# Optimization experiments

Hardware: AMD Instinct MI355X
Metric: run time of the kernel (lower is better)

The kernel has to match this reference:

```python
import jax, jax.numpy as jnp
import numpy as np

GD, LD, HEAD, P, K = 64, 64, 8, 8, 3
GH = HEAD * GD // (GD + LD)   # 4 global heads
LH = HEAD - GH                # 4 local heads
CG = GD // GH                 # 16 = global head dim
CL = LD // LH                 # 16 = local per-head channels
C = GD + LD
EPS = 1e-5


def setup_inputs() -> dict:
    key = jax.random.key(0)
    ks = jax.random.split(key, 16)
    s = 0.02
    inp = {
        'x': jax.random.normal(ks[0], (32, C, 64, 64), jnp.float32),
        'norm_g': jnp.ones((C,), jnp.float32),
        'norm_b': jnp.zeros((C,), jnp.float32),
        'fc1_w': jax.random.normal(ks[1], (3 * GD, GD), jnp.float32) * s,
        'fc1_b': jnp.zeros((3 * GD,), jnp.float32),
        'fc2_w': jax.random.normal(ks[2], (3 * LD, LD), jnp.float32) * s,
        'fc2_b': jnp.zeros((3 * LD,), jnp.float32),
        'qconv_w': jax.random.normal(ks[3], (CL, 1, K, K), jnp.float32) * s,
        'qconv_b': jnp.zeros((CL,), jnp.float32),
        'kconv_w': jax.random.normal(ks[4], (CL, 1, K, K), jnp.float32) * s,
        'kconv_b': jnp.zeros((CL,), jnp.float32),
        'vconv_w': jax.random.normal(ks[5], (CL, 1, K, K), jnp.float32) * s,
        'vconv_b': jnp.zeros((CL,), jnp.float32),
        'fc3_w': jax.random.normal(ks[6], (CL, CL), jnp.float32) * s,
        'fc3_b': jnp.zeros((CL,), jnp.float32),
        'fc4_w': jax.random.normal(ks[7], (CL, CL), jnp.float32) * s,
        'fc4_b': jnp.zeros((CL,), jnp.float32),
        'fc5_w': jax.random.normal(ks[8], (C, C), jnp.float32) * s,
        'fc5_b': jnp.zeros((C,), jnp.float32),
    }
    return inp


def _layernorm(x, g, b):
    m = x.mean(-1, keepdims=True)
    v = ((x - m) ** 2).mean(-1, keepdims=True)
    return (x - m) / jnp.sqrt(v + EPS) * g + b


def _dwconv(x, w, b):
    # x: [N, CL, H, W], w: [CL, 1, K, K] depthwise
    y = jax.lax.conv_general_dilated(
        x, w, (1, 1), [(K // 2, K // 2), (K // 2, K // 2)],
        dimension_numbers=('NCHW', 'OIHW', 'NCHW'), feature_group_count=w.shape[0])
    return y + b[None, :, None, None]


def _conv1x1(x, w, b):
    return jnp.einsum('oc,bchw->bohw', w, x) + b[None, :, None, None]


def reference(x, norm_g, norm_b, fc1_w, fc1_b, fc2_w, fc2_b,
              qconv_w, qconv_b, kconv_w, kconv_b, vconv_w, vconv_b,
              fc3_w, fc3_b, fc4_w, fc4_b, fc5_w, fc5_b):
    B, Cc, H, W = x.shape
    N = H * W
    xn = x.transpose(0, 2, 3, 1).reshape(B, N, Cc)          # b (h w) c
    xn = _layernorm(xn, norm_g, norm_b)
    x_local, x_global = xn[..., :LD], xn[..., LD:]

    # ----- global branch: pooled-KV softmax attention -----
    gqkv = x_global @ fc1_w.T + fc1_b                        # [B,N,3GD]
    gqkv = gqkv.reshape(B, N, 3, GH, CG).transpose(2, 0, 3, 1, 4)  # [3,B,GH,N,CG]
    gq, gk, gv = gqkv[0], gqkv[1], gqkv[2]

    def pool_kv(t):
        t = t.reshape(B, GH, H, W, CG).transpose(0, 1, 4, 2, 3)      # [B,GH,CG,H,W]
        t = t.reshape(B, GH, CG, H // P, P, W // P, P).mean((4, 6))  # avg-pool P
        return t.transpose(0, 1, 3, 4, 2).reshape(B, GH, (H // P) * (W // P), CG)

    gk, gv = pool_kv(gk), pool_kv(gv)
    attn = jnp.einsum('bhnc,bhmc->bhnm', gq, gk) * (GD ** -0.5)  # [B,GH,N,Np]
    attn = jax.nn.softmax(attn, axis=-1)
    xg = jnp.einsum('bhnm,bhmc->bhnc', attn, gv)
    xg = xg.reshape(B, GH, H, W, CG).transpose(0, 1, 4, 2, 3).reshape(B, GD, H, W)

    # ----- local branch: depthwise-conv QKV with swish/tanh gating -----
    lqkv = x_local @ fc2_w.T + fc2_b                          # [B,N,3LD]
    lqkv = lqkv.reshape(B, H, W, 3, LH, CL).transpose(3, 0, 4, 5, 1, 2)
    lqkv = lqkv.reshape(3, B * LH, CL, H, W)
    lq = _dwconv(lqkv[0], qconv_w, qconv_b)
    lk = _dwconv(lqkv[1], kconv_w, kconv_b)
    lv = _dwconv(lqkv[2], vconv_w, vconv_b)
    a = lq * lk
    a = _conv1x1(a, fc3_w, fc3_b)
    a = jax.nn.silu(a)
    a = _conv1x1(a, fc4_w, fc4_b)
    a = jnp.tanh(a / (LD ** -0.5))
    xl = (a * lv).reshape(B, LD, H, W)

    xc = jnp.concatenate([xl, xg], axis=1)                    # [B,C,H,W]
    out = x + _conv1x1(xc, fc5_w, fc5_b)
    return out
```

## Files before the change

### kernel.cpp

```cpp
#include <hip/hip_runtime.h>
#include <cstddef>

#define HW 4096
#define PL 4752
#define RS 72
#define APL (2048 * 4752)

typedef short bf16x8 __attribute__((ext_vector_type(8)));
typedef unsigned short u16x8 __attribute__((ext_vector_type(8)));
typedef float f32x4 __attribute__((ext_vector_type(4)));
typedef unsigned int u32x4 __attribute__((ext_vector_type(4)));
typedef unsigned int u32x2 __attribute__((ext_vector_type(2)));

__device__ __forceinline__ unsigned short f2bf(float f) {
    unsigned u = __builtin_bit_cast(unsigned, f);
    u += 0x7fffu + ((u >> 16) & 1u);
    return (unsigned short)(u >> 16);
}
__device__ __forceinline__ float bf2f(unsigned short s) {
    return __builtin_bit_cast(float, ((unsigned)s) << 16);
}
__device__ __forceinline__ float dpp_left(float x) {
    return __builtin_bit_cast(float,
        __builtin_amdgcn_update_dpp(0, __builtin_bit_cast(int, x), 0x138, 0xf, 0xf, false));
}
__device__ __forceinline__ float dpp_right(float x) {
    return __builtin_bit_cast(float,
        __builtin_amdgcn_update_dpp(0, __builtin_bit_cast(int, x), 0x130, 0xf, 0xf, false));
}

__global__ __launch_bounds__(256) void kprep(
    const float* __restrict__ w1, const float* __restrict__ w2, const float* __restrict__ w5,
    const float* __restrict__ b1, const float* __restrict__ b2,
    unsigned short* __restrict__ wcat, unsigned short* __restrict__ wb5,
    float* __restrict__ bcat)
{
    const int i = blockIdx.x * 256 + threadIdx.x;
    if (i < 384 * 64) {
        const int r = i >> 6;
        wcat[i] = f2bf(r < 192 ? w2[i] : w1[i - 192 * 64]);
    }
    if (i < 128 * 128) wb5[i] = f2bf(w5[i]);
    if (i < 384) bcat[i] = (i < 192) ? b2[i] : b1[i - 192];
}

__global__ __launch_bounds__(256) void kzero(unsigned short* __restrict__ lqkv)
{
    unsigned short* plane = lqkv + (size_t)blockIdx.x * PL;
    const int i = threadIdx.x;
    if (i < 144) {
        const int r = (i < 72) ? 0 : 65;
        plane[r * RS + (i % 72)] = 0;
    }
}

__global__ __launch_bounds__(256) void k1_ln_fc(
    const float* __restrict__ x, const float* __restrict__ ng, const float* __restrict__ nb,
    const unsigned short* __restrict__ wcat, const float* __restrict__ bcat,
    unsigned short* __restrict__ gqb, float* __restrict__ gkp, float* __restrict__ gvp,
    unsigned short* __restrict__ lqkv)
{
    __shared__ unsigned short xnT[64 * 128];
    __shared__ float red[2][4][64];
    const int t = threadIdx.x;
    const int g = t >> 6;
    const int p = t & 63;
    const int bx = blockIdx.x;
    const int b = bx >> 6;
    const int h = bx & 63;
    const float* xrow = x + (size_t)b * 128 * HW + h * 64;

    float v[32];
    float s1 = 0.f, s2 = 0.f;
    #pragma unroll
    for (int i = 0; i < 32; ++i) {
        const int c = g * 32 + i;
        const float vv = xrow[(size_t)c * HW + p];
        v[i] = vv; s1 += vv; s2 += vv * vv;
    }
    red[0][g][p] = s1; red[1][g][p] = s2;
    __syncthreads();
    const float m   = (red[0][0][p] + red[0][1][p] + red[0][2][p] + red[0][3][p]) * (1.f / 128.f);
    const float var = (red[1][0][p] + red[1][1][p] + red[1][2][p] + red[1][3][p]) * (1.f / 128.f) - m * m;
    const float rstd = rsqrtf(var + 1e-5f);

    #pragma unroll
    for (int j = 0; j < 4; ++j) {
        u32x4 pk;
        #pragma unroll
        for (int q = 0; q < 4; ++q) {
            const int i0 = j * 8 + q * 2;
            const int c0 = g * 32 + i0;
            const float f0 = (v[i0]     - m) * rstd * ng[c0]     + nb[c0];
            const float f1 = (v[i0 + 1] - m) * rstd * ng[c0 + 1] + nb[c0 + 1];
            pk[q] = (unsigned)f2bf(f0) | ((unsigned)f2bf(f1) << 16);
        }
        const int colu = (g * 32 + j * 8) ^ ((p & 7) * 8);
        *reinterpret_cast<u32x4*>(&xnT[p * 128 + colu]) = pk;
    }
    __syncthreads();

    const int wid = g;
    const int lg = p >> 4, lr = p & 15;
    const int kbase = (wid >= 2) ? 64 : 0;

    bf16x8 afr[4][2];
    #pragma unroll
    for (int mt = 0; mt < 4; ++mt)
        #pragma unroll
        for (int kc = 0; kc < 2; ++kc) {
            const int pix = mt * 16 + lr;
            const int colu = (kbase + kc * 32 + lg * 8) ^ ((pix & 7) * 8);
            afr[mt][kc] = *reinterpret_cast<const bf16x8*>(&xnT[pix * 128 + colu]);
        }

    const int nbase = wid * 96;
    #pragma unroll
    for (int nt = 0; nt < 6; ++nt) {
        const int o0 = nbase + nt * 16;
        const int o  = o0 + lr;
        const float bias = bcat[o];
        f32x4 acc[4];
        #pragma unroll
        for (int mt = 0; mt < 4; ++mt) acc[mt] = f32x4{bias, bias, bias, bias};
        #pragma unroll
        for (int kc = 0; kc < 2; ++kc) {
            const bf16x8 bfr = *reinterpret_cast<const bf16x8*>(&wcat[(size_t)o * 64 + kc * 32 + lg * 8]);
            #pragma unroll
            for (int mt = 0; mt < 4; ++mt)
                acc[mt] = __builtin_amdgcn_mfma_f32_16x16x32_bf16(afr[mt][kc], bfr, acc[mt], 0, 0, 0);
        }
        if (o0 < 192) {
            const int cc = o0 >> 6;
            const int lh2 = (o0 & 63) >> 4;
            unsigned short* dst = lqkv + (size_t)cc * APL
                                + (((size_t)b * 4 + lh2) * 16 + lr) * PL
                                + (size_t)(h + 1) * RS + 4;
            #pragma unroll
            for (int mt = 0; mt < 4; ++mt) {
                u32x2 pk;
                pk[0] = (unsigned)f2bf(acc[mt][0]) | ((unsigned)f2bf(acc[mt][1]) << 16);
                pk[1] = (unsigned)f2bf(acc[mt][2]) | ((unsigned)f2bf(acc[mt][3]) << 16);
                *reinterpret_cast<u32x2*>(&dst[mt * 16 + lg * 4]) = pk;
            }
        } else if (o0 < 256) {
            const int gh = (o0 - 192) >> 4;
            unsigned short* dst = gqb + (((size_t)b * 4 + gh) * 16) * HW;
            #pragma unroll
            for (int mt = 0; mt < 4; ++mt) {
                u32x2 pk;
                pk[0] = (unsigned)f2bf(acc[mt][0]) | ((unsigned)f2bf(acc[mt][1]) << 16);
                pk[1] = (unsigned)f2bf(acc[mt][2]) | ((unsigned)f2bf(acc[mt][3]) << 16);
                *reinterpret_cast<u32x2*>(&dst[(size_t)lr * HW + h * 64 + mt * 16 + lg * 4]) = pk;
            }
        } else {
            const int kvsel = (o0 - 256) >> 6;
            const int gh = ((o0 - 256) & 63) >> 4;
            float* dst = (kvsel ? gvp : gkp) + (((size_t)b * 4 + gh) * 64 + (h >> 3) * 8) * 16;
            #pragma unroll
            for (int mt = 0; mt < 4; ++mt) {
                float s = acc[mt][0] + acc[mt][1] + acc[mt][2] + acc[mt][3];
                s += __shfl_xor(s, 16);
                if (!(p & 16))
                    atomicAdd(&dst[(2 * mt + (lg >> 1)) * 16 + lr], s * (1.f / 64.f));
            }
        }
    }
}

__global__ __launch_bounds__(256) void k2_attn(
    const unsigned short* __restrict__ gqb, const float* __restrict__ gkp,
    const float* __restrict__ gvp, unsigned short* __restrict__ xc)
{
    __shared__ float skv[2][64][16];
    const int t = threadIdx.x;
    const int bx = blockIdx.x;
    const int tile = bx & 15;
    const int bg = bx >> 4;
    const int b = bg >> 2;
    const int gh = bg & 3;
    for (int i = t; i < 1024; i += 256) {
        skv[0][i >> 4][i & 15] = gkp[(size_t)bg * 1024 + i];
        skv[1][i >> 4][i & 15] = gvp[(size_t)bg * 1024 + i];
    }
    __syncthreads();
    const int n = tile * 256 + t;
    const unsigned short* qp = gqb + (size_t)bg * 16 * HW + n;
    float q[16];
    #pragma unroll
    for (int cg = 0; cg < 16; ++cg) q[cg] = bf2f(qp[(size_t)cg * HW]) * 0.125f;
    float s[64];
    #pragma unroll
    for (int mm = 0; mm < 64; ++mm) {
        float a = 0.f;
        #pragma unroll
        for (int cg = 0; cg < 16; ++cg) a = fmaf(q[cg], skv[0][mm][cg], a);
        s[mm] = a;
    }
    float mx = s[0];
    #pragma unroll
    for (int mm = 1; mm < 64; ++mm) mx = fmaxf(mx, s[mm]);
    float sum = 0.f;
    #pragma unroll
    for (int mm = 0; mm < 64; ++mm) { float e = __expf(s[mm] - mx); s[mm] = e; sum += e; }
    const float rs = 1.f / sum;
    float acc[16];
    #pragma unroll
    for (int cg = 0; cg < 16; ++cg) acc[cg] = 0.f;
    #pragma unroll
    for (int mm = 0; mm < 64; ++mm) {
        const float pm = s[mm];
        #pragma unroll
        for (int cg = 0; cg < 16; ++cg) acc[cg] = fmaf(pm, skv[1][mm][cg], acc[cg]);
    }
    unsigned short* op = xc + ((size_t)b * 128 + 64 + gh * 16) * HW + n;
    #pragma unroll
    for (int cg = 0; cg < 16; ++cg) op[(size_t)cg * HW] = f2bf(acc[cg] * rs);
}

__global__ __launch_bounds__(256, 4) void k3_local(
    const unsigned short* __restrict__ lqkv,
    const float* __restrict__ qw, const float* __restrict__ qb,
    const float* __restrict__ kw, const float* __restrict__ kb,
    const float* __restrict__ vw, const float* __restrict__ vb,
    const float* __restrict__ w3, const float* __restrict__ b3,
    const float* __restrict__ w4, const float* __restrict__ b4,
    unsigned short* __restrict__ xc)
{
    const int t = threadIdx.x;
    const int w = t & 63;
    const int rr = t >> 6;
    const int bx = blockIdx.x;
    const int htile = bx & 15;
    const int bl = bx >> 4;
    const int b = bl >> 2;
    const int lh = bl & 3;
    const int h = htile * 4 + rr;

    float a[16], lvv[16];
    #pragma unroll
    for (int cl = 0; cl < 16; ++cl) {
        const size_t pb = ((size_t)bl * 16 + cl) * PL + (size_t)h * RS + 4 + w;
        float aq = qb[cl], ak = kb[cl], av = vb[cl];
        #pragma unroll
        for (int dy = 0; dy < 3; ++dy) {
            const size_t idx = pb + (size_t)dy * RS;
            const float cq = bf2f(lqkv[idx]);
            const float ck = bf2f(lqkv[idx + APL]);
            const float cv = bf2f(lqkv[idx + 2 * APL]);
            const float lq = dpp_left(cq),  rq = dpp_right(cq);
            const float lk = dpp_left(ck),  rk = dpp_right(ck);
            const float lv = dpp_left(cv),  rv = dpp_right(cv);
            const int wi = cl * 9 + dy * 3;
            aq = fmaf(qw[wi], lq, aq); aq = fmaf(qw[wi + 1], cq, aq); aq = fmaf(qw[wi + 2], rq, aq);
            ak = fmaf(kw[wi], lk, ak); ak = fmaf(kw[wi + 1], ck, ak); ak = fmaf(kw[wi + 2], rk, ak);
            av = fmaf(vw[wi], lv, av); av = fmaf(vw[wi + 1], cv, av); av = fmaf(vw[wi + 2], rv, av);
        }
        a[cl] = aq * ak;
        lvv[cl] = av;
    }

    float a2[16];
    #pragma unroll
    for (int o = 0; o < 16; ++o) {
        float acc = b3[o];
        #pragma unroll
        for (int c2 = 0; c2 < 16; ++c2) acc = fmaf(w3[o * 16 + c2], a[c2], acc);
        a2[o] = acc / (1.f + __expf(-acc));
    }
    unsigned short* op = xc + ((size_t)b * 128 + lh * 16) * HW + (size_t)h * 64 + w;
    #pragma unroll
    for (int o = 0; o < 16; ++o) {
        float acc = b4[o];
        #pragma unroll
        for (int c2 = 0; c2 < 16; ++c2) acc = fmaf(w4[o * 16 + c2], a2[c2], acc);
        const float z = acc * 8.f;
        const float e2 = __expf(-2.f * fabsf(z));
        float th = (1.f - e2) / (1.f + e2);
        th = copysignf(th, z);
        op[(size_t)o * HW] = f2bf(th * lvv[o]);
    }
}

__global__ __launch_bounds__(256) void k4_fc5(
    const float* __restrict__ x, const unsigned short* __restrict__ xc,
    const unsigned short* __restrict__ wb5,
    const float* __restrict__ b5, float* __restrict__ out)
{
    __shared__ unsigned short xcT[64 * 128];
    const int t = threadIdx.x;
    const int g = t >> 6, p = t & 63;
    const int bx = blockIdx.x;
    const int b = bx >> 6, h = bx & 63;
    const unsigned short* cbase = xc + (size_t)b * 128 * HW + h * 64;

    unsigned short vv[32];
    #pragma unroll
    for (int i = 0; i < 32; ++i) vv[i] = cbase[(size_t)(g * 32 + i) * HW + p];
    #pragma unroll
    for (int j = 0; j < 4; ++j) {
        u32x4 pk;
        #pragma unroll
        for (int q = 0; q < 4; ++q) {
            const int i0 = j * 8 + q * 2;
            pk[q] = (unsigned)vv[i0] | ((unsigned)vv[i0 + 1] << 16);
        }
        const int colu = (g * 32 + j * 8) ^ ((p & 7) * 8);
        *reinterpret_cast<u32x4*>(&xcT[p * 128 + colu]) = pk;
    }
    __syncthreads();

    const int wid = g, lg = p >> 4, lr = p & 15;
    bf16x8 afr[4][4];
    #pragma unroll
    for (int mt = 0; mt < 4; ++mt)
        #pragma unroll
        for (int kc = 0; kc < 4; ++kc) {
            const int pix = mt * 16 + lr;
            const int colu = (kc * 32 + lg * 8) ^ ((pix & 7) * 8);
            afr[mt][kc] = *reinterpret_cast<const bf16x8*>(&xcT[pix * 128 + colu]);
        }
    const float* xrow = x + (size_t)b * 128 * HW + h * 64;
    float* obase = out + (size_t)b * 128 * HW + h * 64;
    #pragma unroll
    for (int nt = 0; nt < 2; ++nt) {
        const int o = wid * 32 + nt * 16 + lr;
        const float bias = b5[o];
        f32x4 acc[4];
        #pragma unroll
        for (int mt = 0; mt < 4; ++mt) acc[mt] = f32x4{bias, bias, bias, bias};
        #pragma unroll
        for (int kc = 0; kc < 4; ++kc) {
            const bf16x8 bfr = *reinterpret_cast<const bf16x8*>(&wb5[(size_t)o * 128 + kc * 32 + lg * 8]);
            #pragma unroll
            for (int mt = 0; mt < 4; ++mt)
                acc[mt] = __builtin_amdgcn_mfma_f32_16x16x32_bf16(afr[mt][kc], bfr, acc[mt], 0, 0, 0);
        }
        #pragma unroll
        for (int mt = 0; mt < 4; ++mt) {
            const size_t off = (size_t)o * HW + mt * 16 + lg * 4;
            const f32x4 xr = *reinterpret_cast<const f32x4*>(&xrow[off]);
            const f32x4 r = acc[mt] + xr;
            *reinterpret_cast<f32x4*>(&obase[off]) = r;
        }
    }
}

extern "C" void kernel_launch(void* const* d_in, const int* in_sizes, int n_in,
                              void* d_out, int out_size, void* d_ws, size_t ws_size,
                              hipStream_t stream) {
    const float* x  = (const float*)d_in[0];
    const float* ng = (const float*)d_in[1];
    const float* nb = (const float*)d_in[2];
    const float* w1 = (const float*)d_in[3];
    const float* b1 = (const float*)d_in[4];
    const float* w2 = (const float*)d_in[5];
    const float* b2 = (const float*)d_in[6];
    const float* qw = (const float*)d_in[7];
    const float* qb = (const float*)d_in[8];
    const float* kw = (const float*)d_in[9];
    const float* kb = (const float*)d_in[10];
    const float* vw = (const float*)d_in[11];
    const float* vb = (const float*)d_in[12];
    const float* w3 = (const float*)d_in[13];
    const float* b3 = (const float*)d_in[14];
    const float* w4 = (const float*)d_in[15];
    const float* b4 = (const float*)d_in[16];
    const float* w5 = (const float*)d_in[17];
    const float* b5 = (const float*)d_in[18];
    float* out = (float*)d_out;

    unsigned short* gqb  = (unsigned short*)d_ws;
    float* gkp = (float*)(gqb + 8388608);
    float* gvp = gkp + 131072;
    unsigned short* lqkv = (unsigned short*)(gvp + 131072);
    unsigned short* xc   = lqkv + 3 * APL;
    unsigned short* wcat = xc + 16777216;
    unsigned short* wb5  = wcat + 384 * 64;
    float* bcat = (float*)(wb5 + 128 * 128);

    kprep<<<96, 256, 0, stream>>>(w1, w2, w5, b1, b2, wcat, wb5, bcat);
    kzero<<<6144, 256, 0, stream>>>(lqkv);
    hipMemsetAsync(gkp, 0, 2 * 131072 * sizeof(float), stream);
    k1_ln_fc<<<2048, 256, 0, stream>>>(x, ng, nb, wcat, bcat, gqb, gkp, gvp, lqkv);
    k2_attn<<<2048, 256, 0, stream>>>(gqb, gkp, gvp, xc);
    k3_local<<<2048, 256, 0, stream>>>(lqkv, qw, qb, kw, kb, vw, vb,
                                       w3, b3, w4, b4, xc);
    k4_fc5<<<2048, 256, 0, stream>>>(x, xc, wb5, b5, out);
}
```

Baseline: 301.7 us.

## Store xc pixel-major, drop lqkv row padding, and fold halo zeroing into k1

Measured after the change: 292.0 us. 1.03x faster.

```diff
diff --git a/kernel.cpp b/kernel.cpp
--- a/kernel.cpp
+++ b/kernel.cpp
@@ -2,9 +2,8 @@
 #include <cstddef>
 
 #define HW 4096
-#define PL 4752
-#define RS 72
-#define APL (2048 * 4752)
+#define PL 4224
+#define APL (2048 * 4224)
 
 typedef short bf16x8 __attribute__((ext_vector_type(8)));
 typedef unsigned short u16x8 __attribute__((ext_vector_type(8)));
@@ -44,22 +43,13 @@
     if (i < 384) bcat[i] = (i < 192) ? b2[i] : b1[i - 192];
 }
 
-__global__ __launch_bounds__(256) void kzero(unsigned short* __restrict__ lqkv)
-{
-    unsigned short* plane = lqkv + (size_t)blockIdx.x * PL;
-    const int i = threadIdx.x;
-    if (i < 144) {
-        const int r = (i < 72) ? 0 : 65;
-        plane[r * RS + (i % 72)] = 0;
-    }
-}
-
 __global__ __launch_bounds__(256) void k1_ln_fc(
     const float* __restrict__ x, const float* __restrict__ ng, const float* __restrict__ nb,
     const unsigned short* __restrict__ wcat, const float* __restrict__ bcat,
     unsigned short* __restrict__ gqb, float* __restrict__ gkp, float* __restrict__ gvp,
     unsigned short* __restrict__ lqkv)
 {
+    __shared__ unsigned int xs[128][33];
     __shared__ unsigned short xnT[64 * 128];
     __shared__ float red[2][4][64];
     const int t = threadIdx.x;
@@ -68,14 +58,25 @@
     const int bx = blockIdx.x;
     const int b = bx >> 6;
     const int h = bx & 63;
-    const float* xrow = x + (size_t)b * 128 * HW + h * 64;
+    const float* xbase = x + (size_t)b * 128 * HW + h * 64;
+
+    #pragma unroll
+    for (int i = 0; i < 8; ++i) {
+        const int idx = t + i * 256;
+        const int c = idx >> 4, seg = idx & 15;
+        const f32x4 v4 = *reinterpret_cast<const f32x4*>(&xbase[(size_t)c * HW + seg * 4]);
+        xs[c][seg * 2]     = (unsigned)f2bf(v4[0]) | ((unsigned)f2bf(v4[1]) << 16);
+        xs[c][seg * 2 + 1] = (unsigned)f2bf(v4[2]) | ((unsigned)f2bf(v4[3]) << 16);
+    }
+    __syncthreads();
 
     float v[32];
     float s1 = 0.f, s2 = 0.f;
     #pragma unroll
     for (int i = 0; i < 32; ++i) {
         const int c = g * 32 + i;
-        const float vv = xrow[(size_t)c * HW + p];
+        const unsigned wv = xs[c][p >> 1];
+        const float vv = bf2f((unsigned short)((p & 1) ? (wv >> 16) : (wv & 0xffff)));
         v[i] = vv; s1 += vv; s2 += vv * vv;
     }
     red[0][g][p] = s1; red[1][g][p] = s2;
@@ -135,7 +136,7 @@
             const int lh2 = (o0 & 63) >> 4;
             unsigned short* dst = lqkv + (size_t)cc * APL
                                 + (((size_t)b * 4 + lh2) * 16 + lr) * PL
-                                + (size_t)(h + 1) * RS + 4;
+                                + (size_t)(h + 1) * 64;
             #pragma unroll
             for (int mt = 0; mt < 4; ++mt) {
                 u32x2 pk;
@@ -166,6 +167,17 @@
             }
         }
     }
+
+    if (h == 0 || h == 63) {
+        const size_t rowoff = (h == 0) ? 0 : (size_t)65 * 64;
+        for (int i = t; i < 192 * 8; i += 256) {
+            const int pl2 = i >> 3, sect = i & 7;
+            const int cc = pl2 >> 6, ch = pl2 & 63;
+            const u32x4 z = {0, 0, 0, 0};
+            *reinterpret_cast<u32x4*>(
+                &lqkv[(size_t)cc * APL + ((size_t)b * 64 + ch) * PL + rowoff + sect * 8]) = z;
+        }
+    }
 }
 
 __global__ __launch_bounds__(256) void k2_attn(
@@ -213,9 +225,12 @@
         #pragma unroll
         for (int cg = 0; cg < 16; ++cg) acc[cg] = fmaf(pm, skv[1][mm][cg], acc[cg]);
     }
-    unsigned short* op = xc + ((size_t)b * 128 + 64 + gh * 16) * HW + n;
-    #pragma unroll
-    for (int cg = 0; cg < 16; ++cg) op[(size_t)cg * HW] = f2bf(acc[cg] * rs);
+    unsigned short* op = xc + ((size_t)b * HW + n) * 128 + 64 + gh * 16;
+    u16x8 w0, w1;
+    #pragma unroll
+    for (int j = 0; j < 8; ++j) { w0[j] = f2bf(acc[j] * rs); w1[j] = f2bf(acc[j + 8] * rs); }
+    *reinterpret_cast<u16x8*>(op) = w0;
+    *reinterpret_cast<u16x8*>(op + 8) = w1;
 }
 
 __global__ __launch_bounds__(256, 4) void k3_local(
@@ -240,11 +255,11 @@
     float a[16], lvv[16];
     #pragma unroll
     for (int cl = 0; cl < 16; ++cl) {
-        const size_t pb = ((size_t)bl * 16 + cl) * PL + (size_t)h * RS + 4 + w;
+        const size_t pb = ((size_t)bl * 16 + cl) * PL + (size_t)h * 64 + w;
         float aq = qb[cl], ak = kb[cl], av = vb[cl];
         #pragma unroll
         for (int dy = 0; dy < 3; ++dy) {
-            const size_t idx = pb + (size_t)dy * RS;
+            const size_t idx = pb + (size_t)dy * 64;
             const float cq = bf2f(lqkv[idx]);
             const float ck = bf2f(lqkv[idx + APL]);
             const float cv = bf2f(lqkv[idx + 2 * APL]);
@@ -268,7 +283,7 @@
         for (int c2 = 0; c2 < 16; ++c2) acc = fmaf(w3[o * 16 + c2], a[c2], acc);
         a2[o] = acc / (1.f + __expf(-acc));
     }
-    unsigned short* op = xc + ((size_t)b * 128 + lh * 16) * HW + (size_t)h * 64 + w;
+    u16x8 r0, r1;
     #pragma unroll
     for (int o = 0; o < 16; ++o) {
         float acc = b4[o];
@@ -278,8 +293,12 @@
         const float e2 = __expf(-2.f * fabsf(z));
         float th = (1.f - e2) / (1.f + e2);
         th = copysignf(th, z);
-        op[(size_t)o * HW] = f2bf(th * lvv[o]);
-    }
+        const unsigned short rbf = f2bf(th * lvv[o]);
+        if (o < 8) r0[o] = rbf; else r1[o - 8] = rbf;
+    }
+    unsigned short* op = xc + ((size_t)b * HW + h * 64 + w) * 128 + lh * 16;
+    *reinterpret_cast<u16x8*>(op) = r0;
+    *reinterpret_cast<u16x8*>(op + 8) = r1;
 }
 
 __global__ __launch_bounds__(256) void k4_fc5(
@@ -287,39 +306,21 @@
     const unsigned short* __restrict__ wb5,
     const float* __restrict__ b5, float* __restrict__ out)
 {
-    __shared__ unsigned short xcT[64 * 128];
     const int t = threadIdx.x;
     const int g = t >> 6, p = t & 63;
     const int bx = blockIdx.x;
     const int b = bx >> 6, h = bx & 63;
-    const unsigned short* cbase = xc + (size_t)b * 128 * HW + h * 64;
-
-    unsigned short vv[32];
-    #pragma unroll
-    for (int i = 0; i < 32; ++i) vv[i] = cbase[(size_t)(g * 32 + i) * HW + p];
-    #pragma unroll
-    for (int j = 0; j < 4; ++j) {
-        u32x4 pk;
-        #pragma unroll
-        for (int q = 0; q < 4; ++q) {
-            const int i0 = j * 8 + q * 2;
-            pk[q] = (unsigned)vv[i0] | ((unsigned)vv[i0 + 1] << 16);
-        }
-        const int colu = (g * 32 + j * 8) ^ ((p & 7) * 8);
-        *reinterpret_cast<u32x4*>(&xcT[p * 128 + colu]) = pk;
-    }
-    __syncthreads();
-
     const int wid = g, lg = p >> 4, lr = p & 15;
+
+    const unsigned short* arow = xc + ((size_t)b * HW + h * 64) * 128;
     bf16x8 afr[4][4];
     #pragma unroll
     for (int mt = 0; mt < 4; ++mt)
         #pragma unroll
-        for (int kc = 0; kc < 4; ++kc) {
-            const int pix = mt * 16 + lr;
-            const int colu = (kc * 32 + lg * 8) ^ ((pix & 7) * 8);
-            afr[mt][kc] = *reinterpret_cast<const bf16x8*>(&xcT[pix * 128 + colu]);
-        }
+        for (int kc = 0; kc < 4; ++kc)
+            afr[mt][kc] = *reinterpret_cast<const bf16x8*>(
+                &arow[(size_t)(mt * 16 + lr) * 128 + kc * 32 + lg * 8]);
+
     const float* xrow = x + (size_t)b * 128 * HW + h * 64;
     float* obase = out + (size_t)b * 128 * HW + h * 64;
     #pragma unroll
@@ -380,7 +381,6 @@
     float* bcat = (float*)(wb5 + 128 * 128);
 
     kprep<<<96, 256, 0, stream>>>(w1, w2, w5, b1, b2, wcat, wb5, bcat);
-    kzero<<<6144, 256, 0, stream>>>(lqkv);
     hipMemsetAsync(gkp, 0, 2 * 131072 * sizeof(float), stream);
     k1_ln_fc<<<2048, 256, 0, stream>>>(x, ng, nb, wcat, bcat, gqb, gkp, gvp, lqkv);
     k2_attn<<<2048, 256, 0, stream>>>(gqb, gkp, gvp, xc);
```
